# Kernel optimization log

Measured on AMD Instinct MI355X. Metric: run time of the kernel, lower is better.

Reference implementation:

```python
import jax, jax.numpy as jnp
import numpy as np

PATCH = 4
WINDOW = 4
MAX_ROUNDS = 4
MIN_ROUNDS = 2
LAMBDA_P = 0.2
TOPK = 8


def _ln(x, g, b, eps=1e-5):
    m = x.mean(-1, keepdims=True)
    v = ((x - m) ** 2).mean(-1, keepdims=True)
    return (x - m) / jnp.sqrt(v + eps) * g + b


def _mlp(x, w1, b1, w2, b2):
    # Linear -> exact GELU -> Linear (matches nn.GELU default)
    return jax.nn.gelu(x @ w1 + b1, approximate=False) @ w2 + b2


def setup_inputs() -> dict:
    key = jax.random.key(0)
    ks = jax.random.split(key, 24)
    B, T, D, V = 16, 4096, 256, 256
    s = 0.02
    w = lambda i, shape: jax.random.normal(ks[i], shape, jnp.float32) * s
    z = lambda *shape: jnp.zeros(shape, jnp.float32)
    o = lambda *shape: jnp.ones(shape, jnp.float32)
    return {
        'x': jax.random.randint(ks[0], (B, T), 0, V),
        'emb': w(1, (V, D)), 'pos': w(2, (PATCH, D)),
        'gru_wih': w(3, (D, 3 * D)), 'gru_whh': w(4, (D, 3 * D)),
        'gru_bih': z(3 * D), 'gru_bhh': z(3 * D),
        'ln_p_g': o(D), 'ln_p_b': z(D),
        'sum_w': w(5, (D, D)), 'sum_b': z(D),
        'msg_w1': w(6, (2 * D, D)), 'msg_b1': z(D), 'msg_w2': w(7, (D, D)), 'msg_b2': z(D),
        'upd_w1': w(8, (2 * D, D)), 'upd_b1': z(D), 'upd_w2': w(9, (D, D)), 'upd_b2': z(D),
        'halt_w': w(10, (D, 1)), 'halt_b': z(1),
        'ln_mp_g': o(D), 'ln_mp_b': z(D),
        'q_w': w(11, (D, D)), 'q_b': z(D),
        'k_w': w(12, (D, D)), 'k_b': z(D),
        'v_w': w(13, (D, D)), 'v_b': z(D),
        'o_w': w(14, (D, D)), 'o_b': z(D),
        'bc_w': w(15, (D, D)), 'bc_b': z(D),
        'ln_f_g': o(D), 'ln_f_b': z(D),
        'head_w': w(16, (D, V)),
    }


def reference(x, emb, pos, gru_wih, gru_whh, gru_bih, gru_bhh, ln_p_g, ln_p_b,
              sum_w, sum_b, msg_w1, msg_b1, msg_w2, msg_b2, upd_w1, upd_b1,
              upd_w2, upd_b2, halt_w, halt_b, ln_mp_g, ln_mp_b, q_w, q_b,
              k_w, k_b, v_w, v_b, o_w, o_b, bc_w, bc_b, ln_f_g, ln_f_b, head_w):
    B, T = x.shape
    D = emb.shape[1]
    Np = T // PATCH  # T is divisible by PATCH for these shapes (no pad needed)

    # --- GRU patch processor over B*Np sequences of length PATCH ---
    tok = x.reshape(B * Np, PATCH)
    hseq = emb[tok] + pos[None]  # [BN, P, D]

    def gru_step(h, xt):
        gi = xt @ gru_wih + gru_bih
        gh = h @ gru_whh + gru_bhh
        ir, iz, inn = jnp.split(gi, 3, -1)
        hr, hz, hn = jnp.split(gh, 3, -1)
        r = jax.nn.sigmoid(ir + hr)
        zz = jax.nn.sigmoid(iz + hz)
        n = jnp.tanh(inn + r * hn)
        h = (1 - zz) * n + zz * h
        return h, h

    h0 = jnp.zeros((B * Np, D), hseq.dtype)
    _, gout = jax.lax.scan(gru_step, h0, jnp.swapaxes(hseq, 0, 1))
    local = _ln(jnp.swapaxes(gout, 0, 1), ln_p_g, ln_p_b).reshape(B, Np, PATCH, D)
    summaries = local.mean(2) @ sum_w + sum_b  # [B, Np, D]

    # --- Local message passing with ACT-style halting (fixed MAX_ROUNDS) ---
    h = summaries
    remaining = jnp.ones((B, Np, 1), h.dtype)
    out_mp = jnp.zeros_like(h)
    kl = jnp.zeros((), h.dtype)
    for step in range(MAX_ROUNDS):
        padded = jnp.pad(h, ((0, 0), (WINDOW, 0), (0, 0)))
        # neighbors: self plus previous WINDOW patches -> [B, Np, W+1, D]
        neigh = jnp.stack([padded[:, WINDOW - w:WINDOW - w + Np] for w in range(WINDOW + 1)], axis=2)
        self_exp = jnp.broadcast_to(h[:, :, None, :], neigh.shape)
        msgs = _mlp(jnp.concatenate([self_exp, neigh], -1), msg_w1, msg_b1, msg_w2, msg_b2).mean(2)
        h = _ln(h + _mlp(jnp.concatenate([h, msgs], -1), upd_w1, upd_b1, upd_w2, upd_b2), ln_mp_g, ln_mp_b)
        if step < MIN_ROUNDS:
            hp = jnp.zeros((B, Np, 1), h.dtype)
        else:
            hp = jax.nn.sigmoid(h.mean(1, keepdims=True) @ halt_w + halt_b)  # [B,1,1]
            hp = jnp.broadcast_to(hp, (B, Np, 1))
        if step == MAX_ROUNDS - 1:
            hp = jnp.ones_like(hp)
        out_mp = out_mp + remaining * hp * h
        remaining = remaining * (1 - hp)
        p_geom = LAMBDA_P * (1 - LAMBDA_P) ** step
        # F.kl_div(log(mean+eps), log(p_geom), log_target=True) = p*(log p - log(mean+eps))
        kl = kl + p_geom * (np.log(p_geom) - jnp.log(hp.mean() + 1e-8))
    kl = kl / MAX_ROUNDS

    # --- Sparse top-k causal retrieval ---
    q = out_mp @ q_w + q_b
    kk = out_mp @ k_w + k_b
    v = out_mp @ v_w + v_b
    scores = jnp.einsum('bnd,bmd->bnm', q, kk) / np.sqrt(D).astype(np.float32)
    causal = jnp.tril(jnp.ones((Np, Np), bool))
    neg = jnp.asarray(-jnp.inf, scores.dtype)
    scores = jnp.where(causal[None], scores, neg)
    vals, idx = jax.lax.top_k(scores, TOPK)  # [B, Np, k]
    bi = jnp.arange(B)[:, None, None]
    ni = jnp.arange(Np)[None, :, None]
    sparse = jnp.full_like(scores, neg).at[bi, ni, idx].set(vals)
    attn = jax.nn.softmax(sparse, axis=-1)
    retrieved = jnp.einsum('bnm,bmd->bnd', attn, v) @ o_w + o_b

    # --- Broadcast back to tokens and project ---
    combined = out_mp + retrieved
    broad = combined @ bc_w + bc_b
    final = (local + broad[:, :, None, :]).reshape(B, Np * PATCH, D)[:, :T]
    logits = _ln(final, ln_f_g, ln_f_b) @ head_w
    return logits, kl
```

## Files before the change

### kernel.cpp

```cpp
#include <hip/hip_runtime.h>
#include <math.h>


typedef __bf16 bf16_t;
typedef bf16_t bf16x8 __attribute__((ext_vector_type(8)));
typedef bf16_t bf16x4 __attribute__((ext_vector_type(4)));
typedef float f32x4 __attribute__((ext_vector_type(4)));

#define GF_BIAS 1
#define GF_GELU 4
#define GF_RES 8
#define GF_F32OUT 32

__device__ __forceinline__ float gelu_exact(float x) {
  return 0.5f * x * (1.0f + erff(x * 0.7071067811865475f));
}

__device__ __forceinline__ float sigm(float x) { return 1.f / (1.f + expf(-x)); }

__device__ __forceinline__ float wave_sum(float v) {
#pragma unroll
  for (int o = 32; o; o >>= 1) v += __shfl_xor(v, o, 64);
  return v;
}

__device__ __forceinline__ void gload16(const void* g, void* l) {
  __builtin_amdgcn_global_load_lds(
      (const __attribute__((address_space(1))) void*)g,
      (__attribute__((address_space(3))) void*)l, 16, 0, 0);
}

__device__ __forceinline__ unsigned long long skey(float s, int m) {
  unsigned u = __float_as_uint(s);
  u ^= (u & 0x80000000u) ? 0xFFFFFFFFu : 0x80000000u;
  return ((unsigned long long)u << 32) | (unsigned)(0x7FFFFFFF - m);
}

template<int FLAGS>
__global__ __launch_bounds__(256)
void gemm_bt(const bf16_t* __restrict__ A, const bf16_t* __restrict__ Bt,
             void* __restrict__ Cv, const float* __restrict__ bias,
             const bf16_t* __restrict__ res,
             int lda, int ldb, int ldc, int ldr)
{
  __shared__ __align__(16) bf16_t As[128][64];
  __shared__ __align__(16) bf16_t Bs[128][64];
  const int m0 = blockIdx.x * 128, n0 = blockIdx.y * 128;
  const int tid = threadIdx.x, lane = tid & 63, wave = tid >> 6;
  const int wm = (wave >> 1) << 6, wn = (wave & 1) << 6;
  const int lr = lane & 15, lg = lane >> 4;
  const int cx = lane & 7;

  const int srow = wave * 32 + (lane >> 3);
  const int scol = (((lane & 7) ^ ((lane >> 3) & 7)) * 8);
  const bf16_t* ga = A  + (long long)(m0 + srow) * lda + scol;
  const bf16_t* gb = Bt + (long long)(n0 + srow) * ldb + scol;
  char* lA = (char*)(&As[srow][0]) + (lane & 7) * 16;
  char* lB = (char*)(&Bs[srow][0]) + (lane & 7) * 16;

  f32x4 acc[4][4] = {};

#pragma unroll
  for (int kt = 0; kt < 4; kt++) {
    const int ko = kt * 64;
#pragma unroll
    for (int q = 0; q < 4; q++) {
      gload16(ga + (long long)q * 8 * lda + ko, lA + q * 1024);
      gload16(gb + (long long)q * 8 * ldb + ko, lB + q * 1024);
    }
    __syncthreads();
#pragma unroll
    for (int kk = 0; kk < 2; kk++) {
      const int co = ((kk * 4 + lg) ^ cx) << 4;
      bf16x8 af[4], bfv[4];
#pragma unroll
      for (int i = 0; i < 4; i++)
        af[i]  = *(const bf16x8*)((char*)As + (wm + i * 16 + lr) * 128 + co);
#pragma unroll
      for (int j = 0; j < 4; j++)
        bfv[j] = *(const bf16x8*)((char*)Bs + (wn + j * 16 + lr) * 128 + co);
#pragma unroll
      for (int i = 0; i < 4; i++)
#pragma unroll
        for (int j = 0; j < 4; j++)
          acc[i][j] = __builtin_amdgcn_mfma_f32_16x16x32_bf16(af[i], bfv[j], acc[i][j], 0, 0, 0);
    }
    if (kt < 3) __syncthreads();
  }

#pragma unroll
  for (int i = 0; i < 4; i++) {
#pragma unroll
    for (int j = 0; j < 4; j++) {
      const int col = n0 + wn + j * 16 + lr;
      const float bval = (FLAGS & GF_BIAS) ? bias[col] : 0.f;
#pragma unroll
      for (int e = 0; e < 4; e++) {
        const int row = m0 + wm + i * 16 + lg * 4 + e;
        float v = acc[i][j][e] + bval;
        if (FLAGS & GF_RES) v += (float)res[(long long)row * ldr + col];
        if (FLAGS & GF_GELU) v = gelu_exact(v);
        const long long ci = (long long)row * ldc + col;
        if (FLAGS & GF_F32OUT) ((float*)Cv)[ci] = v;
        else                   ((bf16_t*)Cv)[ci] = (bf16_t)v;
      }
    }
  }
}

template<int FLAGS>
__global__ __launch_bounds__(256)
void gemm64(const bf16_t* __restrict__ A, const bf16_t* __restrict__ Bt,
            void* __restrict__ Cv, const float* __restrict__ bias,
            const bf16_t* __restrict__ res,
            int lda, int ldb, int ldc, int ldr)
{
  __shared__ __align__(16) bf16_t As[64][64];
  __shared__ __align__(16) bf16_t Bs[64][64];
  const int m0 = blockIdx.x * 64, n0 = blockIdx.y * 64;
  const int tid = threadIdx.x, lane = tid & 63, wave = tid >> 6;
  const int wm = (wave >> 1) * 32, wn = (wave & 1) * 32;
  const int lr = lane & 15, lg = lane >> 4;
  const int cx = lane & 7;

  const int srow = tid >> 3;
  const int scol = (((tid & 7) ^ (srow & 7)) * 8);
  const bf16_t* ga = A  + (long long)(m0 + srow) * lda + scol;
  const bf16_t* gb = Bt + (long long)(n0 + srow) * ldb + scol;
  char* lA = (char*)As + tid * 16;
  char* lB = (char*)Bs + tid * 16;

  f32x4 acc[2][2] = {};

#pragma unroll
  for (int kt = 0; kt < 4; kt++) {
    const int ko = kt * 64;
    gload16(ga + ko, lA);
    gload16(ga + 32LL * lda + ko, lA + 4096);
    gload16(gb + ko, lB);
    gload16(gb + 32LL * ldb + ko, lB + 4096);
    __syncthreads();
#pragma unroll
    for (int kk = 0; kk < 2; kk++) {
      const int co = ((kk * 4 + lg) ^ cx) << 4;
      bf16x8 af[2], bfv[2];
#pragma unroll
      for (int i = 0; i < 2; i++)
        af[i]  = *(const bf16x8*)((char*)As + (wm + i * 16 + lr) * 128 + co);
#pragma unroll
      for (int j = 0; j < 2; j++)
        bfv[j] = *(const bf16x8*)((char*)Bs + (wn + j * 16 + lr) * 128 + co);
#pragma unroll
      for (int i = 0; i < 2; i++)
#pragma unroll
        for (int j = 0; j < 2; j++)
          acc[i][j] = __builtin_amdgcn_mfma_f32_16x16x32_bf16(af[i], bfv[j], acc[i][j], 0, 0, 0);
    }
    if (kt < 3) __syncthreads();
  }

#pragma unroll
  for (int i = 0; i < 2; i++) {
#pragma unroll
    for (int j = 0; j < 2; j++) {
      const int col = n0 + wn + j * 16 + lr;
      const float bval = (FLAGS & GF_BIAS) ? bias[col] : 0.f;
#pragma unroll
      for (int e = 0; e < 4; e++) {
        const int row = m0 + wm + i * 16 + lg * 4 + e;
        float v = acc[i][j][e] + bval;
        if (FLAGS & GF_RES) v += (float)res[(long long)row * ldr + col];
        if (FLAGS & GF_GELU) v = gelu_exact(v);
        const long long ci = (long long)row * ldc + col;
        if (FLAGS & GF_F32OUT) ((float*)Cv)[ci] = v;
        else                   ((bf16_t*)Cv)[ci] = (bf16_t)v;
      }
    }
  }
}

__global__ __launch_bounds__(256)
void gemm64_k512(const bf16_t* __restrict__ A1, const bf16_t* __restrict__ A2,
                 const bf16_t* __restrict__ Bt1, const bf16_t* __restrict__ Bt2,
                 bf16_t* __restrict__ C, const float* __restrict__ bias)
{
  __shared__ __align__(16) bf16_t As[64][64];
  __shared__ __align__(16) bf16_t Bs[64][64];
  const int m0 = blockIdx.x * 64, n0 = blockIdx.y * 64;
  const int tid = threadIdx.x, lane = tid & 63, wave = tid >> 6;
  const int wm = (wave >> 1) * 32, wn = (wave & 1) * 32;
  const int lr = lane & 15, lg = lane >> 4;
  const int cx = lane & 7;

  const int srow = tid >> 3;
  const int scol = (((tid & 7) ^ (srow & 7)) * 8);
  char* lA = (char*)As + tid * 16;
  char* lB = (char*)Bs + tid * 16;

  f32x4 acc[2][2] = {};

#pragma unroll
  for (int kt = 0; kt < 8; kt++) {
    const bf16_t* Ap  = (kt < 4) ? A1 : A2;
    const bf16_t* Btp = (kt < 4) ? Bt1 : Bt2;
    const int ko = (kt & 3) * 64;
    const bf16_t* ga = Ap  + (long long)(m0 + srow) * 256 + scol + ko;
    const bf16_t* gb = Btp + (long long)(n0 + srow) * 256 + scol + ko;
    gload16(ga, lA);
    gload16(ga + 32LL * 256, lA + 4096);
    gload16(gb, lB);
    gload16(gb + 32LL * 256, lB + 4096);
    __syncthreads();
#pragma unroll
    for (int kk = 0; kk < 2; kk++) {
      const int co = ((kk * 4 + lg) ^ cx) << 4;
      bf16x8 af[2], bfv[2];
#pragma unroll
      for (int i = 0; i < 2; i++)
        af[i]  = *(const bf16x8*)((char*)As + (wm + i * 16 + lr) * 128 + co);
#pragma unroll
      for (int j = 0; j < 2; j++)
        bfv[j] = *(const bf16x8*)((char*)Bs + (wn + j * 16 + lr) * 128 + co);
#pragma unroll
      for (int i = 0; i < 2; i++)
#pragma unroll
        for (int j = 0; j < 2; j++)
          acc[i][j] = __builtin_amdgcn_mfma_f32_16x16x32_bf16(af[i], bfv[j], acc[i][j], 0, 0, 0);
    }
    if (kt < 7) __syncthreads();
  }

#pragma unroll
  for (int i = 0; i < 2; i++) {
#pragma unroll
    for (int j = 0; j < 2; j++) {
      const int col = n0 + wn + j * 16 + lr;
      const float bval = bias[col];
#pragma unroll
      for (int e = 0; e < 4; e++) {
        const int row = m0 + wm + i * 16 + lg * 4 + e;
        C[(long long)row * 256 + col] = (bf16_t)gelu_exact(acc[i][j][e] + bval);
      }
    }
  }
}

template<int MODE>
__global__ __launch_bounds__(256)
void gemm_ln(const bf16_t* __restrict__ A, const bf16_t* __restrict__ Bt,
             bf16_t* __restrict__ C, const float* __restrict__ bias,
             const float* __restrict__ g, const float* __restrict__ bvec,
             bf16_t* __restrict__ OUTMP, const float* __restrict__ HP)
{
  __shared__ __align__(16) bf16_t As[64][64];
  __shared__ __align__(16) bf16_t Bs[256][64];
  __shared__ float redsum[4][64];
  __shared__ float redsq[4][64];
  const int m0 = blockIdx.x * 64;
  const int tid = threadIdx.x, lane = tid & 63, w = tid >> 6;
  const int lr = lane & 15, lg = lane >> 4, cx = lane & 7;

  f32x4 acc[4][4] = {};

#pragma unroll
  for (int kt = 0; kt < 4; kt++) {
    const int ko = kt * 64;
    {
      int cid = tid, r = cid >> 3, c = cid & 7;
      gload16(A + (long long)(m0 + r) * 256 + ko + ((c ^ (r & 7)) * 8), (char*)As + cid * 16);
      cid = tid + 256; r = cid >> 3; c = cid & 7;
      gload16(A + (long long)(m0 + r) * 256 + ko + ((c ^ (r & 7)) * 8), (char*)As + cid * 16);
    }
#pragma unroll
    for (int it = 0; it < 8; it++) {
      const int cid = it * 256 + tid, r = cid >> 3, c = cid & 7;
      gload16(Bt + (long long)r * 256 + ko + ((c ^ (r & 7)) * 8), (char*)Bs + cid * 16);
    }
    __syncthreads();
#pragma unroll
    for (int kk = 0; kk < 2; kk++) {
      const int co = ((kk * 4 + lg) ^ cx) << 4;
      bf16x8 af[4], bfv[4];
#pragma unroll
      for (int i = 0; i < 4; i++)
        af[i]  = *(const bf16x8*)((char*)As + (i * 16 + lr) * 128 + co);
#pragma unroll
      for (int j = 0; j < 4; j++)
        bfv[j] = *(const bf16x8*)((char*)Bs + (w * 64 + j * 16 + lr) * 128 + co);
#pragma unroll
      for (int i = 0; i < 4; i++)
#pragma unroll
        for (int j = 0; j < 4; j++)
          acc[i][j] = __builtin_amdgcn_mfma_f32_16x16x32_bf16(af[i], bfv[j], acc[i][j], 0, 0, 0);
    }
    if (kt < 3) __syncthreads();
  }

  float v[4][4][4];
  float rs[4][4], rq[4][4];
#pragma unroll
  for (int i = 0; i < 4; i++) {
#pragma unroll
    for (int e = 0; e < 4; e++) { rs[i][e] = 0.f; rq[i][e] = 0.f; }
  }
#pragma unroll
  for (int i = 0; i < 4; i++) {
#pragma unroll
    for (int j = 0; j < 4; j++) {
      const int col = w * 64 + j * 16 + lr;
      const float bval = bias[col];
#pragma unroll
      for (int e = 0; e < 4; e++) {
        const long long rg = m0 + i * 16 + lg * 4 + e;
        const float val = acc[i][j][e] + bval + (float)C[rg * 256 + col];
        v[i][j][e] = val;
        rs[i][e] += val;
        rq[i][e] += val * val;
      }
    }
  }
#pragma unroll
  for (int off = 1; off < 16; off <<= 1) {
#pragma unroll
    for (int i = 0; i < 4; i++)
#pragma unroll
      for (int e = 0; e < 4; e++) {
        rs[i][e] += __shfl_xor(rs[i][e], off, 64);
        rq[i][e] += __shfl_xor(rq[i][e], off, 64);
      }
  }
  if (lr == 0) {
#pragma unroll
    for (int i = 0; i < 4; i++)
#pragma unroll
      for (int e = 0; e < 4; e++) {
        redsum[w][i * 16 + lg * 4 + e] = rs[i][e];
        redsq[w][i * 16 + lg * 4 + e]  = rq[i][e];
      }
  }
  __syncthreads();
  float mean[4][4], rstd[4][4];
#pragma unroll
  for (int i = 0; i < 4; i++) {
#pragma unroll
    for (int e = 0; e < 4; e++) {
      const int r = i * 16 + lg * 4 + e;
      const float S = redsum[0][r] + redsum[1][r] + redsum[2][r] + redsum[3][r];
      const float Q = redsq[0][r] + redsq[1][r] + redsq[2][r] + redsq[3][r];
      const float m = S * (1.f / 256.f);
      float var = Q * (1.f / 256.f) - m * m;
      if (var < 0.f) var = 0.f;
      mean[i][e] = m;
      rstd[i][e] = rsqrtf(var + 1e-5f);
    }
  }
#pragma unroll
  for (int i = 0; i < 4; i++) {
#pragma unroll
    for (int j = 0; j < 4; j++) {
      const int col = w * 64 + j * 16 + lr;
      const float gg = g[col], bb = bvec[col];
#pragma unroll
      for (int e = 0; e < 4; e++) {
        const long long rg = m0 + i * 16 + lg * 4 + e;
        const float y = (v[i][j][e] - mean[i][e]) * rstd[i][e] * gg + bb;
        if (MODE == 0) {
          C[rg * 256 + col] = (bf16_t)y;
        } else {
          const float rem = 1.f - HP[(int)(rg >> 10)];
          OUTMP[rg * 256 + col] = (bf16_t)((float)OUTMP[rg * 256 + col] + rem * y);
        }
      }
    }
  }
}

__global__ __launch_bounds__(256)
void k_fatopk(const bf16_t* __restrict__ QKV, bf16_t* __restrict__ O) {
  __shared__ unsigned long long cand[4][16][8];
  __shared__ float wrow[16][8];
  __shared__ int   irow[16][8];
  const int b = blockIdx.y;
  const int qw = (int)((blockIdx.x + ((unsigned)(b * 21) & 63u)) & 63u);
  const int tid = threadIdx.x;
  const int wid = tid >> 6;
  const int lane = tid & 63;
  const int lr = lane & 15, lg = lane >> 4;
  const bf16_t* Qp = QKV + (long long)b * (1024LL * 768);
  const bf16_t* Kp = Qp + 256;
  const bf16_t* Vp = Qp + 512;
  const int q0 = qw * 16;
  const int qrow = q0 + lr;

  bf16x8 bq[8];
#pragma unroll
  for (int s = 0; s < 8; s++)
    bq[s] = *(const bf16x8*)(Qp + (long long)qrow * 768 + s * 32 + lg * 8);

  unsigned long long kv[8] = {0ull, 0ull, 0ull, 0ull, 0ull, 0ull, 0ull, 0ull};

#define INS8(KEY) {                                                     \
    const unsigned long long k_ = (KEY);                                \
    if (k_ > kv[7]) {                                                   \
      kv[7] = k_;                                                       \
      _Pragma("unroll")                                                 \
      for (int j_ = 7; j_ > 0; j_--)                                    \
        if (kv[j_] > kv[j_-1]) {                                        \
          const unsigned long long t_ = kv[j_];                         \
          kv[j_] = kv[j_-1]; kv[j_-1] = t_;                             \
        }                                                               \
    }                                                                   \
  }

  const int klim = qw + 1;
  for (int base = wid * 2; base < klim; base += 8) {
    const bool hasB = (base + 1 < klim);
    const int ktB = hasB ? base + 1 : base;
    const bf16_t* ka = Kp + (long long)(base * 16 + lr) * 768 + lg * 8;
    const bf16_t* kb = Kp + (long long)(ktB * 16 + lr) * 768 + lg * 8;
    bf16x8 afA[8], afB[8];
#pragma unroll
    for (int s = 0; s < 8; s++) afA[s] = *(const bf16x8*)(ka + s * 32);
#pragma unroll
    for (int s = 0; s < 8; s++) afB[s] = *(const bf16x8*)(kb + s * 32);
    f32x4 a0 = {}, a1 = {}, b0 = {}, b1 = {};
    __builtin_amdgcn_s_setprio(1);
#pragma unroll
    for (int s = 0; s < 8; s += 2) {
      a0 = __builtin_amdgcn_mfma_f32_16x16x32_bf16(afA[s],     bq[s],     a0, 0, 0, 0);
      a1 = __builtin_amdgcn_mfma_f32_16x16x32_bf16(afA[s + 1], bq[s + 1], a1, 0, 0, 0);
      b0 = __builtin_amdgcn_mfma_f32_16x16x32_bf16(afB[s],     bq[s],     b0, 0, 0, 0);
      b1 = __builtin_amdgcn_mfma_f32_16x16x32_bf16(afB[s + 1], bq[s + 1], b1, 0, 0, 0);
    }
    __builtin_amdgcn_s_setprio(0);
#pragma unroll
    for (int e = 0; e < 4; e++) {
      const int m = base * 16 + lg * 4 + e;
      if (m <= qrow) INS8(skey((a0[e] + a1[e]) * 0.0625f, m));
    }
    if (hasB) {
#pragma unroll
      for (int e = 0; e < 4; e++) {
        const int m = ktB * 16 + lg * 4 + e;
        if (m <= qrow) INS8(skey((b0[e] + b1[e]) * 0.0625f, m));
      }
    }
  }
#undef INS8

#pragma unroll
  for (int r = 0; r < 8; r++) {
    unsigned long long mk = kv[0];
    unsigned long long ok = __shfl_xor(mk, 16, 64); if (ok > mk) mk = ok;
    ok = __shfl_xor(mk, 32, 64); if (ok > mk) mk = ok;
    if (lg == 0) cand[wid][lr][r] = mk;
    if (kv[0] == mk && mk != 0ull) {
#pragma unroll
      for (int j = 0; j < 7; j++) kv[j] = kv[j + 1];
      kv[7] = 0ull;
    }
  }
  __syncthreads();

  if (wid == 0) {
    unsigned long long kv2[8];
#pragma unroll
    for (int j = 0; j < 8; j++) kv2[j] = cand[lg][lr][j];
    float wv[8]; int wi[8];
#pragma unroll
    for (int r = 0; r < 8; r++) {
      unsigned long long mk = kv2[0];
      unsigned long long ok = __shfl_xor(mk, 16, 64); if (ok > mk) mk = ok;
      ok = __shfl_xor(mk, 32, 64); if (ok > mk) mk = ok;
      if (mk != 0ull) {
        unsigned hi = (unsigned)(mk >> 32);
        hi ^= (hi & 0x80000000u) ? 0x80000000u : 0xFFFFFFFFu;
        wv[r] = __uint_as_float(hi);
        wi[r] = 0x7FFFFFFF - (int)(unsigned)(mk & 0xFFFFFFFFu);
      } else {
        wv[r] = 0.f; wi[r] = -1;
      }
      if (kv2[0] == mk && mk != 0ull) {
#pragma unroll
        for (int j = 0; j < 7; j++) kv2[j] = kv2[j + 1];
        kv2[7] = 0ull;
      }
    }
    const float mx = wv[0];
    float w8[8]; float den = 0.f;
#pragma unroll
    for (int j = 0; j < 8; j++) {
      w8[j] = (wi[j] >= 0) ? expf(wv[j] - mx) : 0.f;
      den += w8[j];
    }
    const float inv = 1.f / den;
    if (lg == 0) {
#pragma unroll
      for (int j = 0; j < 8; j++) {
        wrow[lr][j] = w8[j] * inv;
        irow[lr][j] = wi[j];
      }
    }
  }
  __syncthreads();

  const int rr = wid * 4 + lg;
  const int c0 = (lane & 15) * 16;
  f32x4 av[4] = {};
#pragma unroll
  for (int j = 0; j < 8; j++) {
    const int idx = irow[rr][j];
    if (idx >= 0) {
      const float wj = wrow[rr][j];
      const bf16_t* vr = Vp + (long long)idx * 768 + c0;
      const bf16x8 v0 = *(const bf16x8*)vr;
      const bf16x8 v1 = *(const bf16x8*)(vr + 8);
#pragma unroll
      for (int e = 0; e < 4; e++) {
        av[0][e] = fmaf(wj, (float)v0[e],     av[0][e]);
        av[1][e] = fmaf(wj, (float)v0[4 + e], av[1][e]);
        av[2][e] = fmaf(wj, (float)v1[e],     av[2][e]);
        av[3][e] = fmaf(wj, (float)v1[4 + e], av[3][e]);
      }
    }
  }
  bf16_t* op = O + ((long long)b * 1024 + q0 + rr) * 256 + c0;
  bf16x8 o0, o1;
#pragma unroll
  for (int e = 0; e < 4; e++) {
    o0[e] = (bf16_t)av[0][e]; o0[4 + e] = (bf16_t)av[1][e];
    o1[e] = (bf16_t)av[2][e]; o1[4 + e] = (bf16_t)av[3][e];
  }
  *(bf16x8*)op = o0;
  *(bf16x8*)(op + 8) = o1;
}

struct TD { const float* src; bf16_t* dst; int N; int k0; int ld; };
struct PrepArgs {
  TD d[16];
  const float* emb; const float* pos; bf16_t* XE;
  const float* msg_b1; const float* msg_b2; const float* upd_w1; const float* upd_b1;
  const float* q_b; const float* k_b; const float* v_b;
  float* BIAS3; float* QKVB;
};

__global__ __launch_bounds__(256) void k_prep(PrepArgs pa) {
  const int y = blockIdx.y, x = blockIdx.x, d = threadIdx.x;
  if (y < 16) {
    TD t = pa.d[y];
    if (x >= t.N) return;
    if (t.k0 < 0) t.dst[(long long)x * 256 + d] = (bf16_t)t.src[(long long)x * t.ld + d];
    else          t.dst[(long long)x * 256 + d] = (bf16_t)t.src[(long long)(t.k0 + d) * t.ld + x];
  } else if (y == 16) {
    const int p = x >> 8, v = x & 255;
    pa.XE[(long long)x * 256 + d] = (bf16_t)(pa.emb[v * 256 + d] + pa.pos[p * 256 + d]);
  } else {
    if      (x == 0) pa.BIAS3[d] = pa.msg_b1[d];
    else if (x == 1) pa.BIAS3[256 + d] = 0.f;
    else if (x == 2) {
      float acc = pa.upd_b1[d];
      for (int k = 0; k < 256; k++) acc += pa.msg_b2[k] * pa.upd_w1[(long long)(256 + k) * 256 + d];
      pa.BIAS3[512 + d] = acc;
    }
    else if (x == 3) pa.QKVB[d] = pa.q_b[d];
    else if (x == 4) pa.QKVB[256 + d] = pa.k_b[d];
    else if (x == 5) pa.QKVB[512 + d] = pa.v_b[d];
  }
}

__global__ __launch_bounds__(256)
void k_gru_gate(const int* __restrict__ x, const bf16_t* __restrict__ gitab,
                const bf16_t* __restrict__ GH, const float* __restrict__ bhh,
                bf16_t* __restrict__ H, bf16_t* __restrict__ LOC, int t)
{
  const int s = blockIdx.x * 4 + (threadIdx.x >> 6);
  const int lane = threadIdx.x & 63, d0 = lane * 4;
  const int v = x[s * 4 + t];
  const bf16_t* gi = gitab + (long long)(t * 256 + v) * 768;
  const bf16x4 g_r = *(const bf16x4*)(gi + d0);
  const bf16x4 g_z = *(const bf16x4*)(gi + 256 + d0);
  const bf16x4 g_n = *(const bf16x4*)(gi + 512 + d0);
  float hr[4], hz[4], hn[4], hp[4];
  if (t == 0) {
#pragma unroll
    for (int e = 0; e < 4; e++) {
      hr[e] = bhh[d0 + e]; hz[e] = bhh[256 + d0 + e]; hn[e] = bhh[512 + d0 + e];
      hp[e] = 0.f;
    }
  } else {
    const bf16_t* gh = GH + (long long)s * 768;
    const bf16x4 a = *(const bf16x4*)(gh + d0);
    const bf16x4 b4 = *(const bf16x4*)(gh + 256 + d0);
    const bf16x4 c4 = *(const bf16x4*)(gh + 512 + d0);
    const bf16x4 hv = *(const bf16x4*)(H + (long long)s * 256 + d0);
#pragma unroll
    for (int e = 0; e < 4; e++) { hr[e] = a[e]; hz[e] = b4[e]; hn[e] = c4[e]; hp[e] = hv[e]; }
  }
  bf16x4 ho;
#pragma unroll
  for (int e = 0; e < 4; e++) {
    const float r = sigm((float)g_r[e] + hr[e]);
    const float zz = sigm((float)g_z[e] + hz[e]);
    const float nn = tanhf((float)g_n[e] + r * hn[e]);
    ho[e] = (bf16_t)((1.f - zz) * nn + zz * hp[e]);
  }
  *(bf16x4*)(H + (long long)s * 256 + d0) = ho;
  *(bf16x4*)(LOC + ((long long)s * 4 + t) * 256 + d0) = ho;
}

__global__ __launch_bounds__(256)
void k_ln(const bf16_t* __restrict__ X, const bf16_t* __restrict__ ADD, int addmode,
          bf16_t* __restrict__ OUT, const float* __restrict__ g,
          const float* __restrict__ b)
{
  const long long r = (long long)blockIdx.x * 4 + (threadIdx.x >> 6);
  const int d0 = (threadIdx.x & 63) * 4;
  const bf16x4 xv = *(const bf16x4*)(X + r * 256 + d0);
  float xf[4];
#pragma unroll
  for (int e = 0; e < 4; e++) xf[e] = (float)xv[e];
  if (addmode == 1) {
    const bf16x4 av = *(const bf16x4*)(ADD + r * 256 + d0);
#pragma unroll
    for (int e = 0; e < 4; e++) xf[e] += (float)av[e];
  } else if (addmode == 2) {
    const bf16x4 av = *(const bf16x4*)(ADD + (r >> 2) * 256 + d0);
#pragma unroll
    for (int e = 0; e < 4; e++) xf[e] += (float)av[e];
  }
  const float mean = wave_sum(xf[0] + xf[1] + xf[2] + xf[3]) * (1.f / 256.f);
  float q = 0.f;
#pragma unroll
  for (int e = 0; e < 4; e++) { const float dx = xf[e] - mean; q += dx * dx; }
  const float rstd = rsqrtf(wave_sum(q) * (1.f / 256.f) + 1e-5f);
  const float4 gv = *(const float4*)(g + d0);
  const float4 bv = *(const float4*)(b + d0);
  const float gg[4] = {gv.x, gv.y, gv.z, gv.w};
  const float bb[4] = {bv.x, bv.y, bv.z, bv.w};
  bf16x4 ov;
#pragma unroll
  for (int e = 0; e < 4; e++) ov[e] = (bf16_t)((xf[e] - mean) * rstd * gg[e] + bb[e]);
  *(bf16x4*)(OUT + r * 256 + d0) = ov;
}

__global__ __launch_bounds__(256)
void k_lnp4(bf16_t* __restrict__ LOC, bf16_t* __restrict__ SUMB,
            const float* __restrict__ g, const float* __restrict__ b)
{
  const long long s = (long long)blockIdx.x * 4 + (threadIdx.x >> 6);
  const int d0 = (threadIdx.x & 63) * 4;
  const float4 gv = *(const float4*)(g + d0);
  const float4 bv = *(const float4*)(b + d0);
  const float gg[4] = {gv.x, gv.y, gv.z, gv.w};
  const float bb[4] = {bv.x, bv.y, bv.z, bv.w};
  float accd[4] = {0.f, 0.f, 0.f, 0.f};
#pragma unroll
  for (int t = 0; t < 4; t++) {
    bf16_t* row = LOC + (s * 4 + t) * 256 + d0;
    const bf16x4 xv = *(const bf16x4*)row;
    float xf[4];
#pragma unroll
    for (int e = 0; e < 4; e++) xf[e] = (float)xv[e];
    const float mean = wave_sum(xf[0] + xf[1] + xf[2] + xf[3]) * (1.f / 256.f);
    float q = 0.f;
#pragma unroll
    for (int e = 0; e < 4; e++) { const float dx = xf[e] - mean; q += dx * dx; }
    const float rstd = rsqrtf(wave_sum(q) * (1.f / 256.f) + 1e-5f);
    bf16x4 ov;
#pragma unroll
    for (int e = 0; e < 4; e++) {
      const float y = (xf[e] - mean) * rstd * gg[e] + bb[e];
      ov[e] = (bf16_t)y;
      accd[e] += y;
    }
    *(bf16x4*)row = ov;
  }
  bf16x4 sv;
#pragma unroll
  for (int e = 0; e < 4; e++) sv[e] = (bf16_t)(accd[e] * 0.25f);
  *(bf16x4*)(SUMB + s * 256 + d0) = sv;
}

__global__ __launch_bounds__(256)
void k_gelumix(const bf16_t* __restrict__ A3, bf16_t* __restrict__ G)
{
  const long long s = (long long)blockIdx.x * 4 + (threadIdx.x >> 6);
  const int n = (int)(s & 1023);
  const int d0 = (threadIdx.x & 63) * 4;
  const bf16x4 av = *(const bf16x4*)(A3 + s * 512 + d0);
  float a[4];
#pragma unroll
  for (int e = 0; e < 4; e++) a[e] = (float)av[e];
  float acc[4] = {0.f, 0.f, 0.f, 0.f};
  const bf16_t* bbase = A3 + s * 512 + 256 + d0;
#pragma unroll
  for (int w = 0; w <= 4; w++) {
    if (n >= w) {
      const bf16x4 bn = *(const bf16x4*)(bbase - (long long)w * 512);
#pragma unroll
      for (int e = 0; e < 4; e++) acc[e] += gelu_exact(a[e] + (float)bn[e]);
    } else {
#pragma unroll
      for (int e = 0; e < 4; e++) acc[e] += gelu_exact(a[e]);
    }
  }
  bf16x4 ov;
#pragma unroll
  for (int e = 0; e < 4; e++) ov[e] = (bf16_t)(acc[e] * 0.2f);
  *(bf16x4*)(G + s * 256 + d0) = ov;
}

__global__ __launch_bounds__(64)
void k_halt1(const bf16_t* __restrict__ Hm, float* __restrict__ PS) {
  const int c = blockIdx.x, b = blockIdx.y, d0 = threadIdx.x * 4;
  float acc[4] = {0.f, 0.f, 0.f, 0.f};
  const bf16_t* base = Hm + ((long long)b * 1024 + c * 32) * 256 + d0;
#pragma unroll 4
  for (int n = 0; n < 32; n++) {
    const bf16x4 hv = *(const bf16x4*)(base + (long long)n * 256);
#pragma unroll
    for (int e = 0; e < 4; e++) acc[e] += (float)hv[e];
  }
  float4 o4; o4.x = acc[0]; o4.y = acc[1]; o4.z = acc[2]; o4.w = acc[3];
  *(float4*)(PS + ((long long)b * 32 + c) * 256 + d0) = o4;
}

__global__ __launch_bounds__(1024)
void k_halt2kl(const float* __restrict__ PS, const float* __restrict__ hw,
               const float* __restrict__ hb, float* __restrict__ HP,
               float* __restrict__ out) {
  __shared__ float sh[16];
  const int b = threadIdx.x >> 6, lane = threadIdx.x & 63, d0 = lane * 4;
  float acc[4] = {0.f, 0.f, 0.f, 0.f};
  for (int c = 0; c < 32; c++) {
    const float4 p4 = *(const float4*)(PS + ((long long)b * 32 + c) * 256 + d0);
    acc[0] += p4.x; acc[1] += p4.y; acc[2] += p4.z; acc[3] += p4.w;
  }
  const float4 w4 = *(const float4*)(hw + d0);
  float val = (acc[0] * w4.x + acc[1] * w4.y + acc[2] * w4.z + acc[3] * w4.w) * (1.f / 1024.f);
  val = wave_sum(val);
  if (lane == 0) {
    const float hp = sigm(val + hb[0]);
    HP[b] = hp;
    sh[b] = hp;
  }
  __syncthreads();
  if (threadIdx.x == 0) {
    float s = 0.f;
    for (int bb = 0; bb < 16; bb++) s += sh[bb];
    const float hpm = s * (1.f / 16.f);
    const float l8 = logf(1e-8f);
    const float p0 = 0.2f, p1 = 0.16f, p2 = 0.128f, p3 = 0.1024f;
    const float kl = p0 * (logf(p0) - l8)
                   + p1 * (logf(p1) - l8)
                   + p2 * (logf(p2) - logf(hpm + 1e-8f))
                   + p3 * (logf(p3) - logf(1.f + 1e-8f));
    out[0] = kl * 0.25f;
  }
}

__global__ __launch_bounds__(256)
void k_outmp(const bf16_t* __restrict__ Hm, const float* __restrict__ HP,
             bf16_t* __restrict__ O) {
  const long long s = (long long)blockIdx.x * 4 + (threadIdx.x >> 6);
  const int d0 = (threadIdx.x & 63) * 4;
  const int b = (int)(s >> 10);
  const float hp = HP[b];
  const bf16x4 hv = *(const bf16x4*)(Hm + s * 256 + d0);
  bf16x4 ov;
#pragma unroll
  for (int e = 0; e < 4; e++) ov[e] = (bf16_t)(hp * (float)hv[e]);
  *(bf16x4*)(O + s * 256 + d0) = ov;
}

extern "C" void kernel_launch(void* const* d_in, const int* in_sizes, int n_in,
                              void* d_out, int out_size, void* d_ws, size_t ws_size,
                              hipStream_t stream) {
  (void)in_sizes; (void)n_in; (void)ws_size;
  const int*   x      = (const int*)d_in[0];
  const float* emb    = (const float*)d_in[1];
  const float* pos    = (const float*)d_in[2];
  const float* wih    = (const float*)d_in[3];
  const float* whh    = (const float*)d_in[4];
  const float* bih    = (const float*)d_in[5];
  const float* bhh    = (const float*)d_in[6];
  const float* lnp_g  = (const float*)d_in[7];
  const float* lnp_b  = (const float*)d_in[8];
  const float* sum_w  = (const float*)d_in[9];
  const float* sum_b  = (const float*)d_in[10];
  const float* msg_w1 = (const float*)d_in[11];
  const float* msg_b1 = (const float*)d_in[12];
  const float* msg_w2 = (const float*)d_in[13];
  const float* msg_b2 = (const float*)d_in[14];
  const float* upd_w1 = (const float*)d_in[15];
  const float* upd_b1 = (const float*)d_in[16];
  const float* upd_w2 = (const float*)d_in[17];
  const float* upd_b2 = (const float*)d_in[18];
  const float* halt_w = (const float*)d_in[19];
  const float* halt_b = (const float*)d_in[20];
  const float* lnm_g  = (const float*)d_in[21];
  const float* lnm_b  = (const float*)d_in[22];
  const float* q_b    = (const float*)d_in[24];
  const float* k_b    = (const float*)d_in[26];
  const float* v_b    = (const float*)d_in[28];
  const float* o_b    = (const float*)d_in[30];
  const float* bc_b   = (const float*)d_in[32];
  const float* lnf_g  = (const float*)d_in[33];
  const float* lnf_b  = (const float*)d_in[34];

  char* base = (char*)d_ws;
  size_t off = 0;
  auto alloc = [&](size_t bytes) -> void* {
    void* p = (void*)(base + off);
    off += (bytes + 255) & ~(size_t)255;
    return p;
  };
  const size_t SL2 = 16384ull * 256 * 2;
  bf16_t* WIHT  = (bf16_t*)alloc(768 * 256 * 2);
  bf16_t* WHHT  = (bf16_t*)alloc(768 * 256 * 2);
  bf16_t* SUMT  = (bf16_t*)alloc(256 * 256 * 2);
  bf16_t* MW    = (bf16_t*)alloc(512 * 256 * 2);
  bf16_t* UW1HT = (bf16_t*)alloc(256 * 256 * 2);
  bf16_t* W2T   = (bf16_t*)alloc(256 * 256 * 2);
  bf16_t* W2NT  = (bf16_t*)alloc(256 * 256 * 2);
  bf16_t* UW1MT = (bf16_t*)alloc(256 * 256 * 2);
  bf16_t* UW2T  = (bf16_t*)alloc(256 * 256 * 2);
  bf16_t* WCB   = (bf16_t*)alloc(256 * 256 * 2);
  bf16_t* QKVW  = (bf16_t*)alloc(768 * 256 * 2);
  bf16_t* OT    = (bf16_t*)alloc(256 * 256 * 2);
  bf16_t* BCT   = (bf16_t*)alloc(256 * 256 * 2);
  bf16_t* HEADT = (bf16_t*)alloc(256 * 256 * 2);
  float*  BIAS3 = (float*)alloc(768 * 4);
  float*  QKVB  = (float*)alloc(768 * 4);
  bf16_t* XE    = (bf16_t*)alloc(1024ull * 256 * 2);
  bf16_t* GITAB = (bf16_t*)alloc(1024ull * 768 * 2);
  bf16_t* LOCb  = (bf16_t*)alloc(65536ull * 256 * 2);

  char*   SCR   = (char*)alloc(16ull * 1024 * 1024 * 4);
  bf16_t* GH    = (bf16_t*)SCR;
  bf16_t* H     = (bf16_t*)(SCR + 25165824);
  bf16_t* SUMB  = (bf16_t*)(SCR + 33554432);
  bf16_t* A3    = (bf16_t*)(SCR + 41943040);

  bf16_t* HMP   = (bf16_t*)alloc(SL2);
  bf16_t* G     = (bf16_t*)alloc(SL2);
  bf16_t* BROAD = (bf16_t*)alloc(SL2);
  bf16_t* UB    = (bf16_t*)alloc(SL2);
  bf16_t* U2B   = (bf16_t*)alloc(SL2);
  bf16_t* OUTMP = (bf16_t*)alloc(SL2);
  bf16_t* QKV   = (bf16_t*)alloc(16384ull * 768 * 2);
  float*  PS    = (float*)alloc(512ull * 256 * 4);
  float*  HP    = (float*)alloc(64);
  bf16_t* ATT   = UB;
  bf16_t* COMB  = U2B;
  float*  out   = (float*)d_out;
  float*  klout = out + (out_size - 1);

  PrepArgs pa;
  pa.d[0]  = { wih,                    WIHT,            768, 0,   768 };
  pa.d[1]  = { whh,                    WHHT,            768, 0,   768 };
  pa.d[2]  = { sum_w,                  SUMT,            256, 0,   256 };
  pa.d[3]  = { msg_w1,                 MW,              256, 0,   256 };
  pa.d[4]  = { msg_w1,                 MW + 256 * 256,  256, 256, 256 };
  pa.d[5]  = { upd_w1,                 UW1HT,           256, 0,   256 };
  pa.d[6]  = { msg_w2,                 W2T,             256, 0,   256 };
  pa.d[7]  = { upd_w1,                 UW1MT,           256, 256, 256 };
  pa.d[8]  = { upd_w2,                 UW2T,            256, 0,   256 };
  pa.d[9]  = { (const float*)d_in[23], QKVW,            256, 0,   256 };
  pa.d[10] = { (const float*)d_in[25], QKVW + 256*256,  256, 0,   256 };
  pa.d[11] = { (const float*)d_in[27], QKVW + 512*256,  256, 0,   256 };
  pa.d[12] = { (const float*)d_in[29], OT,              256, 0,   256 };
  pa.d[13] = { (const float*)d_in[31], BCT,             256, 0,   256 };
  pa.d[14] = { (const float*)d_in[35], HEADT,           256, 0,   256 };
  pa.d[15] = { msg_w2,                 W2NT,            256, -1,  256 };
  pa.emb = emb; pa.pos = pos; pa.XE = XE;
  pa.msg_b1 = msg_b1; pa.msg_b2 = msg_b2; pa.upd_w1 = upd_w1; pa.upd_b1 = upd_b1;
  pa.q_b = q_b; pa.k_b = k_b; pa.v_b = v_b;
  pa.BIAS3 = BIAS3; pa.QKVB = QKVB;
  k_prep<<<dim3(1024, 18), 256, 0, stream>>>(pa);

  gemm64<0><<<dim3(4, 4), 256, 0, stream>>>(
      UW1MT, W2NT, WCB, nullptr, nullptr, 256, 256, 256, 0);

  gemm64<GF_BIAS><<<dim3(16, 12), 256, 0, stream>>>(
      XE, WIHT, GITAB, bih, nullptr, 256, 256, 768, 0);

  k_gru_gate<<<4096, 256, 0, stream>>>(x, GITAB, GH, bhh, H, LOCb, 0);
  for (int t = 1; t < 4; t++) {
    gemm_bt<GF_BIAS><<<dim3(128, 6), 256, 0, stream>>>(
        H, WHHT, GH, bhh, nullptr, 256, 256, 768, 0);
    k_gru_gate<<<4096, 256, 0, stream>>>(x, GITAB, GH, bhh, H, LOCb, t);
  }

  k_lnp4<<<4096, 256, 0, stream>>>(LOCb, SUMB, lnp_g, lnp_b);
  gemm64<GF_BIAS><<<dim3(256, 4), 256, 0, stream>>>(
      SUMB, SUMT, HMP, sum_b, nullptr, 256, 256, 256, 0);

  for (int step = 0; step < 4; step++) {
    gemm_bt<GF_BIAS><<<dim3(128, 4), 256, 0, stream>>>(
        HMP, MW, A3, BIAS3, nullptr, 256, 256, 512, 0);
    k_gelumix<<<4096, 256, 0, stream>>>(A3, G);
    gemm64_k512<<<dim3(256, 4), 256, 0, stream>>>(
        G, HMP, WCB, UW1HT, UB, BIAS3 + 512);
    if (step == 3) {
      gemm_ln<1><<<256, 256, 0, stream>>>(
          UB, UW2T, HMP, upd_b2, lnm_g, lnm_b, OUTMP, HP);
    } else {
      gemm_ln<0><<<256, 256, 0, stream>>>(
          UB, UW2T, HMP, upd_b2, lnm_g, lnm_b, nullptr, nullptr);
      if (step == 2) {
        k_halt1<<<dim3(32, 16), 64, 0, stream>>>(HMP, PS);
        k_halt2kl<<<1, 1024, 0, stream>>>(PS, halt_w, halt_b, HP, klout);
        k_outmp<<<4096, 256, 0, stream>>>(HMP, HP, OUTMP);
      }
    }
  }

  gemm_bt<GF_BIAS><<<dim3(128, 6), 256, 0, stream>>>(
      OUTMP, QKVW, QKV, QKVB, nullptr, 256, 256, 768, 0);
  k_fatopk<<<dim3(64, 16), 256, 0, stream>>>(QKV, ATT);
  gemm64<GF_BIAS | GF_RES><<<dim3(256, 4), 256, 0, stream>>>(
      ATT, OT, COMB, o_b, OUTMP, 256, 256, 256, 256);
  gemm64<GF_BIAS><<<dim3(256, 4), 256, 0, stream>>>(
      COMB, BCT, BROAD, bc_b, nullptr, 256, 256, 256, 0);

  k_ln<<<16384, 256, 0, stream>>>(LOCb, BROAD, 2, LOCb, lnf_g, lnf_b);
  gemm_bt<GF_F32OUT><<<dim3(512, 2), 256, 0, stream>>>(
      LOCb, HEADT, out, nullptr, nullptr, 256, 256, 256, 0);
}
```

Before: 455.7 us.

## Split fused top-k attention into score GEMM plus per-row top-k kernel

```diff
diff --git a/kernel.cpp b/kernel.cpp
--- a/kernel.cpp
+++ b/kernel.cpp
@@ -108,6 +108,76 @@
   }
 }
 
+__global__ __launch_bounds__(256)
+void gemm_sc(const bf16_t* __restrict__ Qb, const bf16_t* __restrict__ Kb,
+             float* __restrict__ S)
+{
+  __shared__ __align__(16) bf16_t As[128][64];
+  __shared__ __align__(16) bf16_t Bs[128][64];
+  const int z = blockIdx.z;
+  const int m0 = blockIdx.x * 128, n0 = blockIdx.y * 128;
+  if (n0 > m0) return;
+  const bf16_t* A  = Qb + (long long)z * (1024LL * 768);
+  const bf16_t* Bt = Kb + (long long)z * (1024LL * 768);
+  float* C = S + (long long)z * (1024LL * 1024);
+  const int tid = threadIdx.x, lane = tid & 63, wave = tid >> 6;
+  const int wm = (wave >> 1) << 6, wn = (wave & 1) << 6;
+  const int lr = lane & 15, lg = lane >> 4;
+  const int cx = lane & 7;
+
+  const int srow = wave * 32 + (lane >> 3);
+  const int scol = (((lane & 7) ^ ((lane >> 3) & 7)) * 8);
+  const bf16_t* ga = A  + (long long)(m0 + srow) * 768 + scol;
+  const bf16_t* gb = Bt + (long long)(n0 + srow) * 768 + scol;
+  char* lA = (char*)(&As[srow][0]) + (lane & 7) * 16;
+  char* lB = (char*)(&Bs[srow][0]) + (lane & 7) * 16;
+
+  f32x4 acc[4][4] = {};
+
+#pragma unroll
+  for (int kt = 0; kt < 4; kt++) {
+    const int ko = kt * 64;
+#pragma unroll
+    for (int q = 0; q < 4; q++) {
+      gload16(ga + (long long)q * 8 * 768 + ko, lA + q * 1024);
+      gload16(gb + (long long)q * 8 * 768 + ko, lB + q * 1024);
+    }
+    __syncthreads();
+#pragma unroll
+    for (int kk = 0; kk < 2; kk++) {
+      const int co = ((kk * 4 + lg) ^ cx) << 4;
+      bf16x8 af[4], bfv[4];
+#pragma unroll
+      for (int i = 0; i < 4; i++)
+        af[i]  = *(const bf16x8*)((char*)As + (wm + i * 16 + lr) * 128 + co);
+#pragma unroll
+      for (int j = 0; j < 4; j++)
+        bfv[j] = *(const bf16x8*)((char*)Bs + (wn + j * 16 + lr) * 128 + co);
+#pragma unroll
+      for (int i = 0; i < 4; i++)
+#pragma unroll
+        for (int j = 0; j < 4; j++)
+          acc[i][j] = __builtin_amdgcn_mfma_f32_16x16x32_bf16(af[i], bfv[j], acc[i][j], 0, 0, 0);
+    }
+    if (kt < 3) __syncthreads();
+  }
+
+#pragma unroll
+  for (int i = 0; i < 4; i++) {
+#pragma unroll
+    for (int j = 0; j < 4; j++) {
+      const int col = n0 + wn + j * 16 + lr;
+#pragma unroll
+      for (int e = 0; e < 4; e++) {
+        const int row = m0 + wm + i * 16 + lg * 4 + e;
+        float v = acc[i][j][e] * 0.0625f;
+        if (col > row) v = -__builtin_inff();
+        C[(long long)row * 1024 + col] = v;
+      }
+    }
+  }
+}
+
 template<int FLAGS>
 __global__ __launch_bounds__(256)
 void gemm64(const bf16_t* __restrict__ A, const bf16_t* __restrict__ Bt,
@@ -376,163 +446,78 @@
 }
 
 __global__ __launch_bounds__(256)
-void k_fatopk(const bf16_t* __restrict__ QKV, bf16_t* __restrict__ O) {
-  __shared__ unsigned long long cand[4][16][8];
-  __shared__ float wrow[16][8];
-  __shared__ int   irow[16][8];
+void k_topk(const float* __restrict__ S, const bf16_t* __restrict__ QKV,
+            bf16_t* __restrict__ O) {
+  const int n = blockIdx.x * 4 + (threadIdx.x >> 6);
   const int b = blockIdx.y;
-  const int qw = (int)((blockIdx.x + ((unsigned)(b * 21) & 63u)) & 63u);
-  const int tid = threadIdx.x;
-  const int wid = tid >> 6;
-  const int lane = tid & 63;
-  const int lr = lane & 15, lg = lane >> 4;
-  const bf16_t* Qp = QKV + (long long)b * (1024LL * 768);
-  const bf16_t* Kp = Qp + 256;
-  const bf16_t* Vp = Qp + 512;
-  const int q0 = qw * 16;
-  const int qrow = q0 + lr;
-
-  bf16x8 bq[8];
-#pragma unroll
-  for (int s = 0; s < 8; s++)
-    bq[s] = *(const bf16x8*)(Qp + (long long)qrow * 768 + s * 32 + lg * 8);
-
-  unsigned long long kv[8] = {0ull, 0ull, 0ull, 0ull, 0ull, 0ull, 0ull, 0ull};
-
-#define INS8(KEY) {                                                     \
-    const unsigned long long k_ = (KEY);                                \
-    if (k_ > kv[7]) {                                                   \
-      kv[7] = k_;                                                       \
-      _Pragma("unroll")                                                 \
-      for (int j_ = 7; j_ > 0; j_--)                                    \
-        if (kv[j_] > kv[j_-1]) {                                        \
-          const unsigned long long t_ = kv[j_];                         \
-          kv[j_] = kv[j_-1]; kv[j_-1] = t_;                             \
-        }                                                               \
-    }                                                                   \
-  }
-
-  const int klim = qw + 1;
-  for (int base = wid * 2; base < klim; base += 8) {
-    const bool hasB = (base + 1 < klim);
-    const int ktB = hasB ? base + 1 : base;
-    const bf16_t* ka = Kp + (long long)(base * 16 + lr) * 768 + lg * 8;
-    const bf16_t* kb = Kp + (long long)(ktB * 16 + lr) * 768 + lg * 8;
-    bf16x8 afA[8], afB[8];
-#pragma unroll
-    for (int s = 0; s < 8; s++) afA[s] = *(const bf16x8*)(ka + s * 32);
-#pragma unroll
-    for (int s = 0; s < 8; s++) afB[s] = *(const bf16x8*)(kb + s * 32);
-    f32x4 a0 = {}, a1 = {}, b0 = {}, b1 = {};
-    __builtin_amdgcn_s_setprio(1);
-#pragma unroll
-    for (int s = 0; s < 8; s += 2) {
-      a0 = __builtin_amdgcn_mfma_f32_16x16x32_bf16(afA[s],     bq[s],     a0, 0, 0, 0);
-      a1 = __builtin_amdgcn_mfma_f32_16x16x32_bf16(afA[s + 1], bq[s + 1], a1, 0, 0, 0);
-      b0 = __builtin_amdgcn_mfma_f32_16x16x32_bf16(afB[s],     bq[s],     b0, 0, 0, 0);
-      b1 = __builtin_amdgcn_mfma_f32_16x16x32_bf16(afB[s + 1], bq[s + 1], b1, 0, 0, 0);
-    }
-    __builtin_amdgcn_s_setprio(0);
-#pragma unroll
-    for (int e = 0; e < 4; e++) {
-      const int m = base * 16 + lg * 4 + e;
-      if (m <= qrow) INS8(skey((a0[e] + a1[e]) * 0.0625f, m));
-    }
-    if (hasB) {
-#pragma unroll
-      for (int e = 0; e < 4; e++) {
-        const int m = ktB * 16 + lg * 4 + e;
-        if (m <= qrow) INS8(skey((b0[e] + b1[e]) * 0.0625f, m));
+  const int lane = threadIdx.x & 63;
+  const float* srow = S + ((long long)(b * 1024 + n)) * 1024;
+  unsigned long long kv[8] = {0, 0, 0, 0, 0, 0, 0, 0};
+  for (int mb = lane * 4; mb <= n; mb += 256) {
+    const float4 s4 = *(const float4*)(srow + mb);
+    const float sv[4] = {s4.x, s4.y, s4.z, s4.w};
+#pragma unroll
+    for (int jj = 0; jj < 4; jj++) {
+      const int m = mb + jj;
+      if (m <= n) {
+        const unsigned long long k = skey(sv[jj], m);
+        if (k > kv[7]) {
+          kv[7] = k;
+#pragma unroll
+          for (int j = 7; j > 0; j--) {
+            if (kv[j] > kv[j-1]) {
+              const unsigned long long t = kv[j]; kv[j] = kv[j-1]; kv[j-1] = t;
+            }
+          }
+        }
       }
     }
   }
-#undef INS8
-
+  float wv[8]; int wi[8];
 #pragma unroll
   for (int r = 0; r < 8; r++) {
     unsigned long long mk = kv[0];
-    unsigned long long ok = __shfl_xor(mk, 16, 64); if (ok > mk) mk = ok;
-    ok = __shfl_xor(mk, 32, 64); if (ok > mk) mk = ok;
-    if (lg == 0) cand[wid][lr][r] = mk;
+#pragma unroll
+    for (int off = 32; off; off >>= 1) {
+      const unsigned long long ok = __shfl_xor(mk, off, 64);
+      if (ok > mk) mk = ok;
+    }
+    if (mk != 0ull) {
+      unsigned hi = (unsigned)(mk >> 32);
+      hi ^= (hi & 0x80000000u) ? 0x80000000u : 0xFFFFFFFFu;
+      wv[r] = __uint_as_float(hi);
+      wi[r] = 0x7FFFFFFF - (int)(unsigned)(mk & 0xFFFFFFFFu);
+    } else {
+      wv[r] = 0.f; wi[r] = -1;
+    }
     if (kv[0] == mk && mk != 0ull) {
 #pragma unroll
       for (int j = 0; j < 7; j++) kv[j] = kv[j + 1];
       kv[7] = 0ull;
     }
   }
-  __syncthreads();
-
-  if (wid == 0) {
-    unsigned long long kv2[8];
-#pragma unroll
-    for (int j = 0; j < 8; j++) kv2[j] = cand[lg][lr][j];
-    float wv[8]; int wi[8];
-#pragma unroll
-    for (int r = 0; r < 8; r++) {
-      unsigned long long mk = kv2[0];
-      unsigned long long ok = __shfl_xor(mk, 16, 64); if (ok > mk) mk = ok;
-      ok = __shfl_xor(mk, 32, 64); if (ok > mk) mk = ok;
-      if (mk != 0ull) {
-        unsigned hi = (unsigned)(mk >> 32);
-        hi ^= (hi & 0x80000000u) ? 0x80000000u : 0xFFFFFFFFu;
-        wv[r] = __uint_as_float(hi);
-        wi[r] = 0x7FFFFFFF - (int)(unsigned)(mk & 0xFFFFFFFFu);
-      } else {
-        wv[r] = 0.f; wi[r] = -1;
-      }
-      if (kv2[0] == mk && mk != 0ull) {
-#pragma unroll
-        for (int j = 0; j < 7; j++) kv2[j] = kv2[j + 1];
-        kv2[7] = 0ull;
-      }
-    }
-    const float mx = wv[0];
-    float w8[8]; float den = 0.f;
-#pragma unroll
-    for (int j = 0; j < 8; j++) {
-      w8[j] = (wi[j] >= 0) ? expf(wv[j] - mx) : 0.f;
-      den += w8[j];
-    }
-    const float inv = 1.f / den;
-    if (lg == 0) {
-#pragma unroll
-      for (int j = 0; j < 8; j++) {
-        wrow[lr][j] = w8[j] * inv;
-        irow[lr][j] = wi[j];
-      }
-    }
-  }
-  __syncthreads();
-
-  const int rr = wid * 4 + lg;
-  const int c0 = (lane & 15) * 16;
-  f32x4 av[4] = {};
+  const float mx = wv[0];
+  float w8[8]; float den = 0.f;
 #pragma unroll
   for (int j = 0; j < 8; j++) {
-    const int idx = irow[rr][j];
-    if (idx >= 0) {
-      const float wj = wrow[rr][j];
-      const bf16_t* vr = Vp + (long long)idx * 768 + c0;
-      const bf16x8 v0 = *(const bf16x8*)vr;
-      const bf16x8 v1 = *(const bf16x8*)(vr + 8);
-#pragma unroll
-      for (int e = 0; e < 4; e++) {
-        av[0][e] = fmaf(wj, (float)v0[e],     av[0][e]);
-        av[1][e] = fmaf(wj, (float)v0[4 + e], av[1][e]);
-        av[2][e] = fmaf(wj, (float)v1[e],     av[2][e]);
-        av[3][e] = fmaf(wj, (float)v1[4 + e], av[3][e]);
-      }
-    }
-  }
-  bf16_t* op = O + ((long long)b * 1024 + q0 + rr) * 256 + c0;
-  bf16x8 o0, o1;
-#pragma unroll
-  for (int e = 0; e < 4; e++) {
-    o0[e] = (bf16_t)av[0][e]; o0[4 + e] = (bf16_t)av[1][e];
-    o1[e] = (bf16_t)av[2][e]; o1[4 + e] = (bf16_t)av[3][e];
-  }
-  *(bf16x8*)op = o0;
-  *(bf16x8*)(op + 8) = o1;
+    w8[j] = (wi[j] >= 0) ? expf(wv[j] - mx) : 0.f;
+    den += w8[j];
+  }
+  const float inv = 1.f / den;
+  float a[4] = {0.f, 0.f, 0.f, 0.f};
+#pragma unroll
+  for (int j = 0; j < 8; j++) {
+    if (wi[j] >= 0) {
+      const bf16x4 vv = *(const bf16x4*)(QKV + ((long long)b * 1024 + wi[j]) * 768 + 512 + lane * 4);
+      const float wj = w8[j] * inv;
+#pragma unroll
+      for (int e = 0; e < 4; e++) a[e] = fmaf(wj, (float)vv[e], a[e]);
+    }
+  }
+  bf16x4 o4;
+#pragma unroll
+  for (int e = 0; e < 4; e++) o4[e] = (bf16_t)a[e];
+  *(bf16x4*)(O + ((long long)(b * 1024 + n)) * 256 + lane * 4) = o4;
 }
 
 struct TD { const float* src; bf16_t* dst; int N; int k0; int ld; };
@@ -837,6 +822,7 @@
   bf16_t* LOCb  = (bf16_t*)alloc(65536ull * 256 * 2);
 
   char*   SCR   = (char*)alloc(16ull * 1024 * 1024 * 4);
+  float*  SCORES = (float*)SCR;
   bf16_t* GH    = (bf16_t*)SCR;
   bf16_t* H     = (bf16_t*)(SCR + 25165824);
   bf16_t* SUMB  = (bf16_t*)(SCR + 33554432);
@@ -918,7 +904,8 @@
 
   gemm_bt<GF_BIAS><<<dim3(128, 6), 256, 0, stream>>>(
       OUTMP, QKVW, QKV, QKVB, nullptr, 256, 256, 768, 0);
-  k_fatopk<<<dim3(64, 16), 256, 0, stream>>>(QKV, ATT);
+  gemm_sc<<<dim3(8, 8, 16), 256, 0, stream>>>(QKV, QKV + 256, SCORES);
+  k_topk<<<dim3(256, 16), 256, 0, stream>>>(SCORES, QKV, ATT);
   gemm64<GF_BIAS | GF_RES><<<dim3(256, 4), 256, 0, stream>>>(
       ATT, OT, COMB, o_b, OUTMP, 256, 256, 256, 256);
   gemm64<GF_BIAS><<<dim3(256, 4), 256, 0, stream>>>(
```

Measured after the change: 457.4 us. Within noise of the previous version (+0.4%).
